# Optimization experiments

Measured on AMD Instinct MI355X. Metric: run time of the kernel, lower is better.

The kernel has to match this reference:

```python
import jax, jax.numpy as jnp
import numpy as np

N = 129  # fixed by fc1: 3*121 -> N-8 = 121
F = 262144
E = 16384

def setup_inputs() -> dict:
    key = jax.random.key(0)
    ks = jax.random.split(key, 18)
    s = 0.05
    return {
        "x": jax.random.normal(ks[0], (N, F), jnp.float32),
        "edge_index": jax.random.randint(ks[1], (2, E), 0, N),
        "edge_attr": jax.random.uniform(ks[2], (E, 3), jnp.float32),
        # GCNConvSortPool (channel1 only; forward reuses it for all 3 edge channels)
        "gcn1_W": jax.random.normal(ks[3], (F, 1), jnp.float32) * (1.0 / np.sqrt(F)),
        "gcn1_b": jnp.zeros((1,), jnp.float32),
        "gcn2_W": jax.random.normal(ks[4], (1, 1), jnp.float32),
        "gcn2_b": jnp.zeros((1,), jnp.float32),
        "conv1_w": jax.random.normal(ks[5], (3, 2, 3), jnp.float32) * s,  # OIH
        "conv1_b": jax.random.normal(ks[6], (3,), jnp.float32) * s,
        "conv2_w": jax.random.normal(ks[7], (1, 3, 3), jnp.float32) * s,
        "conv2_b": jax.random.normal(ks[8], (1,), jnp.float32) * s,
        "fc1_W": jax.random.normal(ks[9], (3 * 121, 32), jnp.float32) * s,
        "fc1_b": jnp.zeros((32,), jnp.float32),
        "fc2_W": jax.random.normal(ks[10], (32, 6), jnp.float32) * s,
        "fc2_b": jnp.zeros((6,), jnp.float32),
        "fc3_W": jax.random.normal(ks[11], (6, 2), jnp.float32) * s,
        "fc3_b": jnp.zeros((2,), jnp.float32),
    }

def _gcn_conv(x, row, col, ew, W, b):
    # PyG GCNConv with edge weights: add self loops (weight 1), symmetric norm.
    n = x.shape[0]
    xw = x @ W                                             # [n, out]
    loop = jnp.arange(n)
    row2 = jnp.concatenate([row, loop])
    col2 = jnp.concatenate([col, loop])
    ew2 = jnp.concatenate([ew, jnp.ones((n,), x.dtype)])
    deg = jax.ops.segment_sum(ew2, col2, num_segments=n)
    dinv = jnp.where(deg > 0, deg ** -0.5, 0.0)
    norm = dinv[row2] * ew2 * dinv[col2]                   # [e+n]
    out = jax.ops.segment_sum(norm[:, None] * xw[row2], col2, num_segments=n)
    return out + b

def _maxpool1d3(z):
    return jax.lax.reduce_window(z, -jnp.inf, jax.lax.max, (1, 1, 3), (1, 1, 1), 'VALID')

def _conv1d(z, w, b):
    out = jax.lax.conv_general_dilated(z, w, (1,), 'VALID', dimension_numbers=('NCH', 'OIH', 'NCH'))
    return out + b[None, :, None]

def _channel(x, row, col, ew, gcn1_W, gcn1_b, gcn2_W, gcn2_b, conv1_w, conv1_b, conv2_w, conv2_b):
    h1 = _gcn_conv(x, row, col, ew, gcn1_W, gcn1_b)        # [N,1]
    h2 = _gcn_conv(h1[:, -1:], row, col, ew, gcn2_W, gcn2_b)  # [N,1]
    h = jnp.concatenate([h1, h2], axis=-1)                 # [N,2]
    perm = jnp.argsort(-h[:, -1])                          # SortPool: sort by last channel, descending, k=N
    h = h[perm]                                            # [N,2]
    z = h.T[None]                                          # [1,2,N]
    z = _maxpool1d3(_conv1d(z, conv1_w, conv1_b))          # [1,3,N-4]
    z = _maxpool1d3(_conv1d(z, conv2_w, conv2_b))          # [1,1,N-8]
    return z

def reference(x, edge_index, edge_attr, gcn1_W, gcn1_b, gcn2_W, gcn2_b,
              conv1_w, conv1_b, conv2_w, conv2_b,
              fc1_W, fc1_b, fc2_W, fc2_b, fc3_W, fc3_b):
    row, col = edge_index[0], edge_index[1]
    outs = [_channel(x, row, col, edge_attr[:, c], gcn1_W, gcn1_b, gcn2_W, gcn2_b,
                     conv1_w, conv1_b, conv2_w, conv2_b) for c in range(3)]
    all_x = jnp.concatenate(outs, axis=-2)                 # [1,3,121]
    h = all_x.reshape(1, -1)                               # [1,363]
    h = jax.nn.elu(h @ fc1_W + fc1_b)                      # dropout=0 -> identity
    h = jax.nn.elu(h @ fc2_W + fc2_b)
    return h @ fc3_W + fc3_b                               # [1,2]
```

## Files before the change

### kernel.cpp

```cpp
#include <hip/hip_runtime.h>
#include <hip/hip_bf16.h>
#include <math.h>

#define NN 129
#define FF 262144
#define EE 16384
#define CHUNKS 32
#define CHUNK (FF / CHUNKS)
#define NB 16
#define EPB (EE / NB)
#define EPT (EPB / 256)

#define OFF_PARTIAL 0
#define OFF_DEGP    (OFF_PARTIAL + NN*CHUNKS)
#define OFF_H1P     (OFF_DEGP + NB*3*NN)
#define OFF_H2P     (OFF_H1P + NB*3*NN)
#define OFF_BAR     (OFF_H2P + NB*3*NN)

typedef float vfloat4 __attribute__((ext_vector_type(4)));

__global__ __launch_bounds__(256) void k_matvec(
    const float* __restrict__ x, const float* __restrict__ W,
    const int* __restrict__ eidx, const float* __restrict__ eattr,
    double* __restrict__ ws)
{
    const int b = blockIdx.x;
    const int tid = threadIdx.x;
    const int wave = tid >> 6, lane = tid & 63;

    __shared__ double ws4[4];
    __shared__ double dp[4][3][NN];

    if (b < NN * CHUNKS) {
        const int r = b / CHUNKS, ch = b % CHUNKS;
        const vfloat4* xp = (const vfloat4*)(x + (size_t)r * FF + (size_t)ch * CHUNK);
        const float4*  wp = (const float4*)(W + (size_t)ch * CHUNK);
        double acc = 0.0;
#pragma unroll
        for (int i = 0; i < CHUNK / (256 * 4); ++i) {
            vfloat4 xv = __builtin_nontemporal_load(xp + tid + i * 256);
            float4  wv = wp[tid + i * 256];
            acc += (double)xv[0] * (double)wv.x + (double)xv[1] * (double)wv.y
                 + (double)xv[2] * (double)wv.z + (double)xv[3] * (double)wv.w;
        }
        for (int off = 32; off > 0; off >>= 1) acc += __shfl_down(acc, off, 64);
        if (lane == 0) ws4[wave] = acc;
        __syncthreads();
        if (tid == 0) ws[OFF_PARTIAL + b] = (ws4[0] + ws4[1]) + (ws4[2] + ws4[3]);
    } else {
        const int bb = b - NN * CHUNKS;
        if (bb == 0 && tid == 0) {
            unsigned* bar = (unsigned*)(ws + OFF_BAR);
            __hip_atomic_store(&bar[0], 0u, __ATOMIC_RELAXED, __HIP_MEMORY_SCOPE_AGENT);
            __hip_atomic_store(&bar[1], 0u, __ATOMIC_RELAXED, __HIP_MEMORY_SCOPE_AGENT);
        }
        for (int i = tid; i < 4 * 3 * NN; i += 256) ((double*)dp)[i] = 0.0;
        __syncthreads();
        const int* col = eidx + EE;
#pragma unroll
        for (int i = 0; i < EPT; ++i) {
            const int e = bb * EPB + i * 256 + tid;
            const int cl = col[e];
#pragma unroll
            for (int c = 0; c < 3; ++c)
                unsafeAtomicAdd(&dp[wave][c][cl], (double)eattr[e * 3 + c]);
        }
        __syncthreads();
        for (int i = tid; i < 3 * NN; i += 256) {
            const int c = i / NN, j = i % NN;
            ws[OFF_DEGP + bb * (3 * NN) + i] =
                (dp[0][c][j] + dp[1][c][j]) + (dp[2][c][j] + dp[3][c][j]);
        }
    }
}

__device__ __forceinline__ void gbar(unsigned* bar, int idx) {
    __syncthreads();
    if (threadIdx.x == 0) {
        __threadfence();
        __hip_atomic_fetch_add(&bar[idx], 1u, __ATOMIC_ACQ_REL, __HIP_MEMORY_SCOPE_AGENT);
        while (__hip_atomic_load(&bar[idx], __ATOMIC_ACQUIRE, __HIP_MEMORY_SCOPE_AGENT) < (unsigned)NB)
            __builtin_amdgcn_s_sleep(1);
        __threadfence();
    }
    __syncthreads();
}

__global__ __launch_bounds__(256) void k_rest(
    const int* __restrict__ eidx, const float* __restrict__ eattr,
    double* __restrict__ ws,
    const float* __restrict__ b1, const float* __restrict__ W2, const float* __restrict__ b2,
    const float* __restrict__ c1w, const float* __restrict__ c1b,
    const float* __restrict__ c2w, const float* __restrict__ c2b,
    const float* __restrict__ f1W, const float* __restrict__ f1b,
    const float* __restrict__ f2W, const float* __restrict__ f2b,
    const float* __restrict__ f3W, const float* __restrict__ f3b,
    float* __restrict__ out)
{
    __shared__ double sxw[NN];
    __shared__ double sdinv[3][NN];
    __shared__ double sh1[3][NN];
    __shared__ double hp[4][3][NN];
    __shared__ double h2f[3][NN];
    __shared__ double z0[3][NN], z1[3][NN];
    __shared__ int    rnk[3][NN];
    __shared__ double c1o[3][3][127];
    __shared__ double p1o[3][3][125];
    __shared__ double c2o[3][123];
    __shared__ double allx[363];
    __shared__ double fc1o[32], fc2o[6];

    const int b = blockIdx.x, tid = threadIdx.x, wave = tid >> 6;
    unsigned* bar = (unsigned*)(ws + OFF_BAR);
    const int* row = eidx;
    const int* col = eidx + EE;

    for (int j = tid; j < NN; j += 256) {
        double s = 0.0;
#pragma unroll
        for (int k = 0; k < CHUNKS; ++k) s += ws[OFF_PARTIAL + j * CHUNKS + k];
        sxw[j] = s;
    }
    for (int v = tid; v < 3 * NN; v += 256) {
        double d = 1.0;
#pragma unroll
        for (int k = 0; k < NB; ++k) d += ws[OFF_DEGP + k * (3 * NN) + v];
        ((double*)sdinv)[v] = (d > 0.0) ? 1.0 / sqrt(d) : 0.0;
    }
    for (int i = tid; i < 4 * 3 * NN; i += 256) ((double*)hp)[i] = 0.0;
    __syncthreads();

    int er[EPT], ec[EPT];
    double enw[EPT][3];
#pragma unroll
    for (int i = 0; i < EPT; ++i) {
        const int e = b * EPB + i * 256 + tid;
        const int r = row[e], cl = col[e];
        er[i] = r; ec[i] = cl;
        const double xwr = sxw[r];
#pragma unroll
        for (int c = 0; c < 3; ++c) {
            const double nw = sdinv[c][r] * (double)eattr[e * 3 + c] * sdinv[c][cl];
            enw[i][c] = nw;
            unsafeAtomicAdd(&hp[wave][c][cl], nw * xwr);
        }
    }
    __syncthreads();
    for (int i = tid; i < 3 * NN; i += 256) {
        const int c = i / NN, j = i % NN;
        ws[OFF_H1P + b * (3 * NN) + i] =
            (hp[0][c][j] + hp[1][c][j]) + (hp[2][c][j] + hp[3][c][j]);
    }
    gbar(bar, 0);

    const double bb1 = (double)b1[0];
    for (int i = tid; i < 3 * NN; i += 256) {
        const int j = i % NN;
        const double dv = ((double*)sdinv)[i];
        double s = dv * dv * sxw[j] + bb1;
#pragma unroll
        for (int k = 0; k < NB; ++k) s += ws[OFF_H1P + k * (3 * NN) + i];
        ((double*)sh1)[i] = s;
    }
    for (int i = tid; i < 4 * 3 * NN; i += 256) ((double*)hp)[i] = 0.0;
    __syncthreads();

    const double w2 = (double)W2[0];
#pragma unroll
    for (int i = 0; i < EPT; ++i) {
        const int r = er[i], cl = ec[i];
#pragma unroll
        for (int c = 0; c < 3; ++c)
            unsafeAtomicAdd(&hp[wave][c][cl], enw[i][c] * (sh1[c][r] * w2));
    }
    __syncthreads();
    for (int i = tid; i < 3 * NN; i += 256) {
        const int c = i / NN, j = i % NN;
        ws[OFF_H2P + b * (3 * NN) + i] =
            (hp[0][c][j] + hp[1][c][j]) + (hp[2][c][j] + hp[3][c][j]);
    }
    gbar(bar, 1);

    if (b != 0) return;

    const double bb2 = (double)b2[0];
    for (int i = tid; i < 3 * NN; i += 256) {
        const int j = i % NN;
        const double dv = ((double*)sdinv)[i];
        double s = dv * dv * (((double*)sh1)[i] * w2) + bb2;
#pragma unroll
        for (int k = 0; k < NB; ++k) s += ws[OFF_H2P + k * (3 * NN) + i];
        ((double*)h2f)[i] = s;
    }
    __syncthreads();

    for (int i = tid; i < 3 * NN; i += 256) {
        const int c = i / NN, j = i % NN;
        const double v = h2f[c][j];
        int rk = 0;
        for (int q = 0; q < NN; ++q) {
            const double u = h2f[c][q];
            rk += (u > v) || (u == v && q < j);
        }
        rnk[c][j] = rk;
    }
    __syncthreads();
    for (int i = tid; i < 3 * NN; i += 256) {
        const int c = i / NN, j = i % NN;
        const int rk = rnk[c][j];
        z0[c][rk] = sh1[c][j];
        z1[c][rk] = h2f[c][j];
    }
    __syncthreads();

    for (int i = tid; i < 3 * 3 * 127; i += 256) {
        const int c = i / (3 * 127), rem = i % (3 * 127), o = rem / 127, p = rem % 127;
        double s = (double)c1b[o];
#pragma unroll
        for (int k = 0; k < 3; ++k) {
            s += (double)c1w[(o * 2 + 0) * 3 + k] * z0[c][p + k];
            s += (double)c1w[(o * 2 + 1) * 3 + k] * z1[c][p + k];
        }
        c1o[c][o][p] = s;
    }
    __syncthreads();
    for (int i = tid; i < 3 * 3 * 125; i += 256) {
        const int c = i / (3 * 125), rem = i % (3 * 125), o = rem / 125, p = rem % 125;
        p1o[c][o][p] = fmax(c1o[c][o][p], fmax(c1o[c][o][p + 1], c1o[c][o][p + 2]));
    }
    __syncthreads();
    for (int i = tid; i < 3 * 123; i += 256) {
        const int c = i / 123, p = i % 123;
        double s = (double)c2b[0];
#pragma unroll
        for (int ic = 0; ic < 3; ++ic)
#pragma unroll
            for (int k = 0; k < 3; ++k)
                s += (double)c2w[ic * 3 + k] * p1o[c][ic][p + k];
        c2o[c][p] = s;
    }
    __syncthreads();
    for (int i = tid; i < 3 * 121; i += 256) {
        const int c = i / 121, p = i % 121;
        allx[c * 121 + p] = fmax(c2o[c][p], fmax(c2o[c][p + 1], c2o[c][p + 2]));
    }
    __syncthreads();

    {
        const int j = tid >> 3, t = tid & 7;
        double s = 0.0;
        for (int i = t; i < 363; i += 8) s += allx[i] * (double)f1W[i * 32 + j];
        s += __shfl_down(s, 4, 8);
        s += __shfl_down(s, 2, 8);
        s += __shfl_down(s, 1, 8);
        if (t == 0) {
            s += (double)f1b[j];
            fc1o[j] = (s > 0.0) ? s : expm1(s);
        }
    }
    __syncthreads();
    if (tid < 6) {
        double s = (double)f2b[tid];
        for (int i = 0; i < 32; ++i) s += fc1o[i] * (double)f2W[i * 6 + tid];
        fc2o[tid] = (s > 0.0) ? s : expm1(s);
    }
    __syncthreads();
    if (tid < 2) {
        double s = (double)f3b[tid];
        for (int i = 0; i < 6; ++i) s += fc2o[i] * (double)f3W[i * 2 + tid];
        out[tid] = (float)s;
    }
}

extern "C" void kernel_launch(void* const* d_in, const int* in_sizes, int n_in,
                              void* d_out, int out_size, void* d_ws, size_t ws_size,
                              hipStream_t stream) {
    const float* x    = (const float*)d_in[0];
    const int*   eidx = (const int*)d_in[1];
    const float* eattr= (const float*)d_in[2];
    const float* g1W  = (const float*)d_in[3];
    const float* g1b  = (const float*)d_in[4];
    const float* g2W  = (const float*)d_in[5];
    const float* g2b  = (const float*)d_in[6];
    const float* c1w  = (const float*)d_in[7];
    const float* c1b  = (const float*)d_in[8];
    const float* c2w  = (const float*)d_in[9];
    const float* c2b  = (const float*)d_in[10];
    const float* f1W  = (const float*)d_in[11];
    const float* f1b  = (const float*)d_in[12];
    const float* f2W  = (const float*)d_in[13];
    const float* f2b  = (const float*)d_in[14];
    const float* f3W  = (const float*)d_in[15];
    const float* f3b  = (const float*)d_in[16];
    float* out = (float*)d_out;
    double* ws = (double*)d_ws;

    k_matvec<<<NN * CHUNKS + NB, 256, 0, stream>>>(x, g1W, eidx, eattr, ws);
    k_rest<<<NB, 256, 0, stream>>>(eidx, eattr, ws,
                                   g1b, g2W, g2b, c1w, c1b, c2w, c2b,
                                   f1W, f1b, f2W, f2b, f3W, f3b, out);
}
```

Measured before the change: 256.0 us.

## Spread edge work across 64 blocks with one edge per thread

Raises the edge-block count from 16 to 64 so each thread handles a single edge, removing the per-thread edge loops and register arrays. Edge loads are hoisted ahead of the shared-memory zeroing. The matvec dot product is split into two accumulators to shorten the dependency chain. In exchange, the grid barrier now spans 64 cooperating blocks and each partial-sum reduction reads 64 partials instead of 16.

```diff
diff --git a/kernel.cpp b/kernel.cpp
--- a/kernel.cpp
+++ b/kernel.cpp
@@ -7,9 +7,8 @@
 #define EE 16384
 #define CHUNKS 32
 #define CHUNK (FF / CHUNKS)
-#define NB 16
+#define NB 64
 #define EPB (EE / NB)
-#define EPT (EPB / 256)
 
 #define OFF_PARTIAL 0
 #define OFF_DEGP    (OFF_PARTIAL + NN*CHUNKS)
@@ -35,14 +34,15 @@
         const int r = b / CHUNKS, ch = b % CHUNKS;
         const vfloat4* xp = (const vfloat4*)(x + (size_t)r * FF + (size_t)ch * CHUNK);
         const float4*  wp = (const float4*)(W + (size_t)ch * CHUNK);
-        double acc = 0.0;
+        double acc0 = 0.0, acc1 = 0.0;
 #pragma unroll
         for (int i = 0; i < CHUNK / (256 * 4); ++i) {
             vfloat4 xv = __builtin_nontemporal_load(xp + tid + i * 256);
             float4  wv = wp[tid + i * 256];
-            acc += (double)xv[0] * (double)wv.x + (double)xv[1] * (double)wv.y
-                 + (double)xv[2] * (double)wv.z + (double)xv[3] * (double)wv.w;
-        }
+            acc0 += (double)xv[0] * (double)wv.x + (double)xv[1] * (double)wv.y;
+            acc1 += (double)xv[2] * (double)wv.z + (double)xv[3] * (double)wv.w;
+        }
+        double acc = acc0 + acc1;
         for (int off = 32; off > 0; off >>= 1) acc += __shfl_down(acc, off, 64);
         if (lane == 0) ws4[wave] = acc;
         __syncthreads();
@@ -54,17 +54,14 @@
             __hip_atomic_store(&bar[0], 0u, __ATOMIC_RELAXED, __HIP_MEMORY_SCOPE_AGENT);
             __hip_atomic_store(&bar[1], 0u, __ATOMIC_RELAXED, __HIP_MEMORY_SCOPE_AGENT);
         }
+        const int e = bb * EPB + tid;
+        const int cl = eidx[EE + e];
+        const float a0 = eattr[e * 3 + 0], a1 = eattr[e * 3 + 1], a2 = eattr[e * 3 + 2];
         for (int i = tid; i < 4 * 3 * NN; i += 256) ((double*)dp)[i] = 0.0;
         __syncthreads();
-        const int* col = eidx + EE;
-#pragma unroll
-        for (int i = 0; i < EPT; ++i) {
-            const int e = bb * EPB + i * 256 + tid;
-            const int cl = col[e];
-#pragma unroll
-            for (int c = 0; c < 3; ++c)
-                unsafeAtomicAdd(&dp[wave][c][cl], (double)eattr[e * 3 + c]);
-        }
+        unsafeAtomicAdd(&dp[wave][0][cl], (double)a0);
+        unsafeAtomicAdd(&dp[wave][1][cl], (double)a1);
+        unsafeAtomicAdd(&dp[wave][2][cl], (double)a2);
         __syncthreads();
         for (int i = tid; i < 3 * NN; i += 256) {
             const int c = i / NN, j = i % NN;
@@ -112,8 +109,13 @@
 
     const int b = blockIdx.x, tid = threadIdx.x, wave = tid >> 6;
     unsigned* bar = (unsigned*)(ws + OFF_BAR);
-    const int* row = eidx;
-    const int* col = eidx + EE;
+
+    const int e = b * EPB + tid;
+    const int er = eidx[e];
+    const int ec = eidx[EE + e];
+    const float ea0 = eattr[e * 3 + 0];
+    const float ea1 = eattr[e * 3 + 1];
+    const float ea2 = eattr[e * 3 + 2];
 
     for (int j = tid; j < NN; j += 256) {
         double s = 0.0;
@@ -123,27 +125,20 @@
     }
     for (int v = tid; v < 3 * NN; v += 256) {
         double d = 1.0;
-#pragma unroll
         for (int k = 0; k < NB; ++k) d += ws[OFF_DEGP + k * (3 * NN) + v];
         ((double*)sdinv)[v] = (d > 0.0) ? 1.0 / sqrt(d) : 0.0;
     }
     for (int i = tid; i < 4 * 3 * NN; i += 256) ((double*)hp)[i] = 0.0;
     __syncthreads();
 
-    int er[EPT], ec[EPT];
-    double enw[EPT][3];
-#pragma unroll
-    for (int i = 0; i < EPT; ++i) {
-        const int e = b * EPB + i * 256 + tid;
-        const int r = row[e], cl = col[e];
-        er[i] = r; ec[i] = cl;
-        const double xwr = sxw[r];
-#pragma unroll
-        for (int c = 0; c < 3; ++c) {
-            const double nw = sdinv[c][r] * (double)eattr[e * 3 + c] * sdinv[c][cl];
-            enw[i][c] = nw;
-            unsafeAtomicAdd(&hp[wave][c][cl], nw * xwr);
-        }
+    double nw0 = sdinv[0][er] * (double)ea0 * sdinv[0][ec];
+    double nw1 = sdinv[1][er] * (double)ea1 * sdinv[1][ec];
+    double nw2 = sdinv[2][er] * (double)ea2 * sdinv[2][ec];
+    {
+        const double xwr = sxw[er];
+        unsafeAtomicAdd(&hp[wave][0][ec], nw0 * xwr);
+        unsafeAtomicAdd(&hp[wave][1][ec], nw1 * xwr);
+        unsafeAtomicAdd(&hp[wave][2][ec], nw2 * xwr);
     }
     __syncthreads();
     for (int i = tid; i < 3 * NN; i += 256) {
@@ -158,7 +153,6 @@
         const int j = i % NN;
         const double dv = ((double*)sdinv)[i];
         double s = dv * dv * sxw[j] + bb1;
-#pragma unroll
         for (int k = 0; k < NB; ++k) s += ws[OFF_H1P + k * (3 * NN) + i];
         ((double*)sh1)[i] = s;
     }
@@ -166,13 +160,9 @@
     __syncthreads();
 
     const double w2 = (double)W2[0];
-#pragma unroll
-    for (int i = 0; i < EPT; ++i) {
-        const int r = er[i], cl = ec[i];
-#pragma unroll
-        for (int c = 0; c < 3; ++c)
-            unsafeAtomicAdd(&hp[wave][c][cl], enw[i][c] * (sh1[c][r] * w2));
-    }
+    unsafeAtomicAdd(&hp[wave][0][ec], nw0 * (sh1[0][er] * w2));
+    unsafeAtomicAdd(&hp[wave][1][ec], nw1 * (sh1[1][er] * w2));
+    unsafeAtomicAdd(&hp[wave][2][ec], nw2 * (sh1[2][er] * w2));
     __syncthreads();
     for (int i = tid; i < 3 * NN; i += 256) {
         const int c = i / NN, j = i % NN;
@@ -188,7 +178,6 @@
         const int j = i % NN;
         const double dv = ((double*)sdinv)[i];
         double s = dv * dv * (((double*)sh1)[i] * w2) + bb2;
-#pragma unroll
         for (int k = 0; k < NB; ++k) s += ws[OFF_H2P + k * (3 * NN) + i];
         ((double*)h2f)[i] = s;
     }
```

Result: slower. 269.4 us (+5.2%).
